# Optimization experiments

Hardware: AMD Instinct MI355X
Metric: run time of the kernel (lower is better)

The kernel has to match this reference:

```python
import jax, jax.numpy as jnp
import numpy as np
import math

HEADS, DIM_HEAD, LANDMARKS, PINV_ITERS = 8, 64, 256, 6
EMB = 512


def layer_norm(x, g, b, eps=1e-5):
    mu = jnp.mean(x, -1, keepdims=True)
    var = jnp.mean((x - mu) ** 2, -1, keepdims=True)
    return (x - mu) / jnp.sqrt(var + eps) * g + b


def moore_penrose_pinv(x, iters=PINV_ITERS):
    # iterative Moore-Penrose pseudo-inverse (lucidrains nystrom-attention)
    abs_x = jnp.abs(x)
    col = abs_x.sum(-1)
    row = abs_x.sum(-2)
    z = jnp.swapaxes(x, -1, -2) / (jnp.max(col) * jnp.max(row))
    I = jnp.eye(x.shape[-1], dtype=x.dtype)
    for _ in range(iters):
        xz = x @ z
        z = 0.25 * z @ (13.0 * I - xz @ (15.0 * I - xz @ (7.0 * I - xz)))
    return z


def dw_seq_conv(v, w):
    # v: [b, h, n, d]; depthwise Conv2d(heads, heads, (33,1), pad (16,0), groups=heads)
    return jax.lax.conv_general_dilated(
        v, w, (1, 1), ((w.shape[2] // 2, w.shape[2] // 2), (0, 0)),
        dimension_numbers=('NCHW', 'OIHW', 'NCHW'), feature_group_count=v.shape[1])


def nystrom_attention(x, qkv_w, out_w, out_b, res_w):
    b, n, _ = x.shape
    m = LANDMARKS
    pad = (m - n % m) % m
    if pad:
        x = jnp.pad(x, ((0, 0), (pad, 0), (0, 0)))  # front-pad like F.pad(..., padding, 0)
    n_p = n + pad
    qkv = x @ qkv_w  # [b, n_p, 3*h*dh]
    q, k, v = jnp.split(qkv, 3, axis=-1)
    to_h = lambda t: t.reshape(b, n_p, HEADS, DIM_HEAD).transpose(0, 2, 1, 3)
    q, k, v = to_h(q), to_h(k), to_h(v)
    q = q * (DIM_HEAD ** -0.5)
    l = n_p // m  # tokens per landmark
    q_l = q.reshape(b, HEADS, m, l, DIM_HEAD).mean(3)
    k_l = k.reshape(b, HEADS, m, l, DIM_HEAD).mean(3)
    a1 = jax.nn.softmax(jnp.einsum('bhid,bhjd->bhij', q, k_l), -1)    # [b,h,n_p,m]
    a2 = jax.nn.softmax(jnp.einsum('bhid,bhjd->bhij', q_l, k_l), -1)  # [b,h,m,m]
    a3 = jax.nn.softmax(jnp.einsum('bhid,bhjd->bhij', q_l, k), -1)    # [b,h,m,n_p]
    a2_inv = moore_penrose_pinv(a2)
    out = (a1 @ a2_inv) @ (a3 @ v)  # [b,h,n_p,dh]
    out = out + dw_seq_conv(v, res_w)  # residual depthwise conv on v
    out = out.transpose(0, 2, 1, 3).reshape(b, n_p, HEADS * DIM_HEAD)
    out = out @ out_w + out_b
    return out[:, -n:]


def ppeg(x, H, W, w7, b7, w5, b5, w3, b3):
    B, _, C = x.shape
    cls_t, feat = x[:, :1], x[:, 1:]
    f = feat.transpose(0, 2, 1).reshape(B, C, H, W)
    def dw(w, b):
        y = jax.lax.conv_general_dilated(
            f, w, (1, 1), 'SAME', dimension_numbers=('NCHW', 'OIHW', 'NCHW'),
            feature_group_count=C)
        return y + b[None, :, None, None]
    y = f + dw(w7, b7) + dw(w5, b5) + dw(w3, b3)
    y = y.reshape(B, C, H * W).transpose(0, 2, 1)
    return jnp.concatenate([cls_t, y], axis=1)


def setup_inputs():
    key = jax.random.key(0)
    ks = jax.random.split(key, 20)
    rn = lambda k, shp, s=0.02: jax.random.normal(k, shp, jnp.float32) * s
    return {
        'x_path': jax.random.normal(ks[0], (4, 6000, 1024), jnp.float32),
        'fc1_w': rn(ks[1], (1024, EMB)), 'fc1_b': jnp.zeros((EMB,), jnp.float32),
        'cls_token': jax.random.normal(ks[2], (1, 1, EMB), jnp.float32),
        'ln1_g': jnp.ones((EMB,), jnp.float32), 'ln1_b': jnp.zeros((EMB,), jnp.float32),
        'qkv1_w': rn(ks[3], (EMB, 3 * HEADS * DIM_HEAD)),
        'out1_w': rn(ks[4], (HEADS * DIM_HEAD, EMB)), 'out1_b': jnp.zeros((EMB,), jnp.float32),
        'res1_w': rn(ks[5], (HEADS, 1, 33, 1)),
        'ln2_g': jnp.ones((EMB,), jnp.float32), 'ln2_b': jnp.zeros((EMB,), jnp.float32),
        'qkv2_w': rn(ks[6], (EMB, 3 * HEADS * DIM_HEAD)),
        'out2_w': rn(ks[7], (HEADS * DIM_HEAD, EMB)), 'out2_b': jnp.zeros((EMB,), jnp.float32),
        'res2_w': rn(ks[8], (HEADS, 1, 33, 1)),
        'conv7_w': rn(ks[9], (EMB, 1, 7, 7)), 'conv7_b': jnp.zeros((EMB,), jnp.float32),
        'conv5_w': rn(ks[10], (EMB, 1, 5, 5)), 'conv5_b': jnp.zeros((EMB,), jnp.float32),
        'conv3_w': rn(ks[11], (EMB, 1, 3, 3)), 'conv3_b': jnp.zeros((EMB,), jnp.float32),
        'norm_g': jnp.ones((EMB,), jnp.float32), 'norm_b': jnp.zeros((EMB,), jnp.float32),
        'fc2_w': rn(ks[12], (EMB, 4)), 'fc2_b': jnp.zeros((4,), jnp.float32),
    }


def reference(x_path, fc1_w, fc1_b, cls_token, ln1_g, ln1_b, qkv1_w, out1_w, out1_b,
              res1_w, ln2_g, ln2_b, qkv2_w, out2_w, out2_b, res2_w,
              conv7_w, conv7_b, conv5_w, conv5_b, conv3_w, conv3_b,
              norm_g, norm_b, fc2_w, fc2_b):
    h = jax.nn.relu(x_path @ fc1_w + fc1_b)  # [B, N, EMB]
    B, N = h.shape[0], h.shape[1]
    _H = int(math.ceil(math.sqrt(N)))
    add = _H * _H - N
    h = jnp.concatenate([h, h[:, :add]], axis=1)            # square padding
    cls = jnp.broadcast_to(cls_token, (B, 1, EMB))
    h = jnp.concatenate([cls, h], axis=1)                   # [B, _H*_H+1, EMB]
    # TransLayer 1
    h = h + nystrom_attention(layer_norm(h, ln1_g, ln1_b), qkv1_w, out1_w, out1_b, res1_w)
    # PPEG positional encoding
    h = ppeg(h, _H, _H, conv7_w, conv7_b, conv5_w, conv5_b, conv3_w, conv3_b)
    # TransLayer 2
    h = h + nystrom_attention(layer_norm(h, ln2_g, ln2_b), qkv2_w, out2_w, out2_b, res2_w)
    h = layer_norm(h, norm_g, norm_b)
    logits = h @ fc2_w + fc2_b
    cls_logit = logits[:, 0]
    Y_hat = jnp.argmax(cls_logit, axis=1)
    hazards = jax.nn.sigmoid(cls_logit)
    S = jnp.cumprod(1.0 - hazards, axis=1)
    return hazards, S, Y_hat
```

## Files before the change

### kernel.cpp

```cpp
#include <hip/hip_runtime.h>
#include <math.h>

namespace {

constexpr int Bq   = 4;
constexpr int N0   = 6000;
constexpr int KIN  = 1024;
constexpr int E    = 512;
constexpr int HH   = 78;
constexpr int HWp  = 6084;
constexpr int N1   = 6085;
constexpr int NH   = 8;
constexpr int DH   = 64;
constexpr int LM   = 256;
constexpr int NP   = 6144;
constexpr int LCH  = 24;
constexpr int PADS = 59;
constexpr int BH   = Bq * NH;
constexpr int QKV  = 3 * E;

typedef __attribute__((ext_vector_type(8))) short bf16x8;
typedef __attribute__((ext_vector_type(4))) float f32x4;

__host__ __device__ inline int gblocks_i(long long n) { return (int)((n + 255) / 256); }

__device__ inline unsigned short f2bf(float x) {
  unsigned u = __float_as_uint(x);
  u += 0x7FFFu + ((u >> 16) & 1u);
  return (unsigned short)(u >> 16);
}
__device__ inline float bf2f(unsigned short s) {
  return __uint_as_float(((unsigned)s) << 16);
}
__device__ inline int swz8(int row, int chunk) {
  return chunk ^ (row & 7) ^ ((row >> 3) & 7);
}

__global__ __launch_bounds__(256)
void wcvt_t(const float* __restrict__ in, unsigned short* __restrict__ out, int K, int N)
{
  __shared__ float T[32][33];
  const int tx = threadIdx.x & 31, ty = threadIdx.x >> 5;
  const int n0 = blockIdx.x * 32, k0 = blockIdx.y * 32;
  #pragma unroll
  for (int i = 0; i < 4; i++)
    T[ty + i * 8][tx] = in[(size_t)(k0 + ty + i * 8) * N + n0 + tx];
  __syncthreads();
  #pragma unroll
  for (int i = 0; i < 4; i++)
    out[(size_t)(n0 + ty + i * 8) * K + k0 + tx] = f2bf(T[tx][ty + i * 8]);
}

template<int ASRC, int STORE, bool BIAS, bool RELU, bool SWIZ>
__global__ __launch_bounds__(256)
void mgemm(const void* __restrict__ Av, const unsigned short* __restrict__ Bt,
           const float* __restrict__ bias, float* __restrict__ C,
           unsigned short* __restrict__ qp, unsigned short* __restrict__ kp,
           unsigned short* __restrict__ vp, const unsigned short* __restrict__ Ag,
           int Mrows, int N, int K)
{
  __shared__ __align__(16) short As[128 * 40];
  __shared__ __align__(16) short Bs[128 * 40];
  const int t = threadIdx.x;
  const int lane = t & 63;
  const int l16 = lane & 15, g = lane >> 4;
  const int wave = t >> 6;
  const int wr = (wave >> 1) * 64, wc = (wave & 1) * 64;

  int bx = blockIdx.x, by = blockIdx.y;
  if (SWIZ) {
    const int gx = gridDim.x, nwg = gx * gridDim.y;
    const int flat = by * gx + bx;
    const int qq = nwg >> 3, rr = nwg & 7;
    const int xcd = flat & 7, pos = flat >> 3;
    const int nid = (xcd < rr ? xcd * (qq + 1) : rr * (qq + 1) + (xcd - rr) * qq) + pos;
    bx = nid % gx; by = nid / gx;
  }
  const int rowBase = by * 128, colBase = bx * 128;

  f32x4 acc[4][4];
  #pragma unroll
  for (int mi = 0; mi < 4; mi++)
    #pragma unroll
    for (int ni = 0; ni < 4; ni++) acc[mi][ni] = (f32x4){0.f, 0.f, 0.f, 0.f};

  for (int k0 = 0; k0 < K; k0 += 32) {
    if (ASRC == 0) {
      const float* A = (const float*)Av;
      #pragma unroll
      for (int i = 0; i < 4; i++) {
        const int id = i * 256 + t;
        const int row = id >> 3, kq = id & 7;
        const int r = rowBase + row;
        float4 va = make_float4(0.f, 0.f, 0.f, 0.f);
        if (r < Mrows)
          va = *reinterpret_cast<const float4*>(A + (size_t)r * K + k0 + kq * 4);
        const unsigned lo = (unsigned)f2bf(va.x) | ((unsigned)f2bf(va.y) << 16);
        const unsigned hi = (unsigned)f2bf(va.z) | ((unsigned)f2bf(va.w) << 16);
        *reinterpret_cast<uint2*>(&As[row * 40 + kq * 4]) = make_uint2(lo, hi);
      }
    } else {
      #pragma unroll
      for (int i = 0; i < 2; i++) {
        const int id = i * 256 + t;
        const int row = id >> 2, c8 = id & 3;
        const int r = rowBase + row;
        int4 va = make_int4(0, 0, 0, 0);
        if (r < Mrows) {
          const int kk = k0 + c8 * 8;
          if (ASRC == 4) {
            const int b = r / N1, rr2 = r % N1;
            va = *reinterpret_cast<const int4*>(
                Ag + (((size_t)(b * NH + (kk >> 6))) * NP + PADS + rr2) * DH + (kk & 63));
          } else {
            va = *reinterpret_cast<const int4*>(((const unsigned short*)Av) + (size_t)r * K + kk);
          }
        }
        *reinterpret_cast<int4*>(&As[row * 40 + c8 * 8]) = va;
      }
    }
    #pragma unroll
    for (int i = 0; i < 2; i++) {
      const int id = i * 256 + t;
      const int row = id >> 2, g8 = id & 3;
      int4 vb = *reinterpret_cast<const int4*>(Bt + (size_t)(colBase + row) * K + k0 + g8 * 8);
      *reinterpret_cast<int4*>(&Bs[row * 40 + g8 * 8]) = vb;
    }
    __syncthreads();
    bf16x8 af[4], bf[4];
    #pragma unroll
    for (int mi = 0; mi < 4; mi++)
      af[mi] = *reinterpret_cast<const bf16x8*>(&As[(wr + mi * 16 + l16) * 40 + g * 8]);
    #pragma unroll
    for (int ni = 0; ni < 4; ni++)
      bf[ni] = *reinterpret_cast<const bf16x8*>(&Bs[(wc + ni * 16 + l16) * 40 + g * 8]);
    #pragma unroll
    for (int mi = 0; mi < 4; mi++)
      #pragma unroll
      for (int ni = 0; ni < 4; ni++)
        acc[mi][ni] = __builtin_amdgcn_mfma_f32_16x16x32_bf16(af[mi], bf[ni], acc[mi][ni], 0, 0, 0);
    __syncthreads();
  }

  #pragma unroll
  for (int mi = 0; mi < 4; mi++) {
    #pragma unroll
    for (int ni = 0; ni < 4; ni++) {
      #pragma unroll
      for (int r4 = 0; r4 < 4; r4++) {
        const int row = rowBase + wr + mi * 16 + g * 4 + r4;
        if (row >= Mrows) continue;
        const int col = colBase + wc + ni * 16 + l16;
        float v = acc[mi][ni][r4];
        if (BIAS) v += bias[col];
        if (RELU) v = fmaxf(v, 0.f);
        if (STORE == 2) {
          const int b   = row / N1;
          const int p   = (row % N1) + PADS;
          const int wch = col >> 9;
          const int hd  = (col >> 6) & 7;
          const int d   = col & 63;
          float vv = (wch == 0) ? v * 0.125f : v;
          unsigned short* dst = (wch == 0) ? qp : (wch == 1) ? kp : vp;
          dst[(((size_t)(b * NH + hd)) * NP + p) * DH + d] = f2bf(vv);
        } else if (STORE == 1) {
          C[((size_t)(row / N0) * N1 + 1 + (row % N0)) * N + col] = v;
        } else if (STORE == 3) {
          C[(size_t)row * N + col] += v;
        } else {
          C[(size_t)row * N + col] = v;
        }
      }
    }
  }
}

template<bool WN, bool WT, bool TBF>
__global__ __launch_bounds__(256)
void mm_ns(const float* __restrict__ A, const float* __restrict__ BT,
           float* __restrict__ Cn, unsigned short* __restrict__ CtB,
           float* __restrict__ CtF, int Ncols, int Mtot, int K,
           long long sA, long long sBT, long long sCn, long long sCt,
           float cN, float aN, float cT, float aT)
{
  const int z = blockIdx.z;
  A  += (size_t)z * sA;
  BT += (size_t)z * sBT;
  __shared__ __align__(16) char smem[32768];
  unsigned short* Ah = (unsigned short*)smem;
  unsigned short* Al = Ah + 4096;
  unsigned short* Bh = Ah + 8192;
  unsigned short* Bl = Ah + 12288;
  const int t = threadIdx.x, lane = t & 63, w = t >> 6;
  const int l15 = lane & 15, g = lane >> 4;
  const int rb = blockIdx.y * 64, cb = blockIdx.x * 64;
  const int wr = w * 16;

  f32x4 acc[4];
  #pragma unroll
  for (int ni = 0; ni < 4; ni++) acc[ni] = (f32x4){0.f, 0.f, 0.f, 0.f};

  for (int k0 = 0; k0 < K; k0 += 64) {
    if (k0) __syncthreads();
    #pragma unroll
    for (int it = 0; it < 4; it++) {
      const int id = it * 256 + t;
      const int row = id >> 4, kq = (id & 15) * 4;
      float4 va = *reinterpret_cast<const float4*>(A + (size_t)(rb + row) * K + k0 + kq);
      const int eo = row * 64 + swz8(row, kq >> 3) * 8 + (kq & 7);
      unsigned short h0 = f2bf(va.x), h1 = f2bf(va.y), h2 = f2bf(va.z), h3 = f2bf(va.w);
      unsigned short lo0 = f2bf(va.x - bf2f(h0)), lo1 = f2bf(va.y - bf2f(h1));
      unsigned short lo2 = f2bf(va.z - bf2f(h2)), lo3 = f2bf(va.w - bf2f(h3));
      *reinterpret_cast<ushort4*>(&Ah[eo]) = make_ushort4(h0, h1, h2, h3);
      *reinterpret_cast<ushort4*>(&Al[eo]) = make_ushort4(lo0, lo1, lo2, lo3);
      float4 vb = *reinterpret_cast<const float4*>(BT + (size_t)(cb + row) * K + k0 + kq);
      unsigned short b0 = f2bf(vb.x), b1 = f2bf(vb.y), b2 = f2bf(vb.z), b3 = f2bf(vb.w);
      unsigned short c0_ = f2bf(vb.x - bf2f(b0)), c1 = f2bf(vb.y - bf2f(b1));
      unsigned short c2 = f2bf(vb.z - bf2f(b2)), c3 = f2bf(vb.w - bf2f(b3));
      *reinterpret_cast<ushort4*>(&Bh[eo]) = make_ushort4(b0, b1, b2, b3);
      *reinterpret_cast<ushort4*>(&Bl[eo]) = make_ushort4(c0_, c1, c2, c3);
    }
    __syncthreads();
    #pragma unroll
    for (int ds = 0; ds < 2; ds++) {
      const int ar = wr + l15;
      bf16x8 ah = *reinterpret_cast<const bf16x8*>(&Ah[ar * 64 + swz8(ar, ds * 4 + g) * 8]);
      bf16x8 al = *reinterpret_cast<const bf16x8*>(&Al[ar * 64 + swz8(ar, ds * 4 + g) * 8]);
      #pragma unroll
      for (int ni = 0; ni < 4; ni++) {
        const int nr = ni * 16 + l15;
        bf16x8 bhf = *reinterpret_cast<const bf16x8*>(&Bh[nr * 64 + swz8(nr, ds * 4 + g) * 8]);
        bf16x8 blf = *reinterpret_cast<const bf16x8*>(&Bl[nr * 64 + swz8(nr, ds * 4 + g) * 8]);
        acc[ni] = __builtin_amdgcn_mfma_f32_16x16x32_bf16(ah, bhf, acc[ni], 0, 0, 0);
        acc[ni] = __builtin_amdgcn_mfma_f32_16x16x32_bf16(ah, blf, acc[ni], 0, 0, 0);
        acc[ni] = __builtin_amdgcn_mfma_f32_16x16x32_bf16(al, bhf, acc[ni], 0, 0, 0);
      }
    }
  }
  __syncthreads();
  float* tb = (float*)smem;
  #pragma unroll
  for (int ni = 0; ni < 4; ni++)
    #pragma unroll
    for (int r = 0; r < 4; r++)
      tb[(wr + g * 4 + r) * 65 + l15 + ni * 16] = acc[ni][r];
  __syncthreads();
  #pragma unroll
  for (int it = 0; it < 4; it++) {
    const int id = it * 256 + t;
    const int row = id >> 4, q4 = (id & 15) * 4;
    if (WN) {
      float4 o;
      #pragma unroll
      for (int j = 0; j < 4; j++) {
        float v = tb[row * 65 + q4 + j];
        ((float*)&o)[j] = ((rb + row) == (cb + q4 + j) ? cN : 0.f) + aN * v;
      }
      *reinterpret_cast<float4*>(Cn + (size_t)z * sCn + (size_t)(rb + row) * Ncols + cb + q4) = o;
    }
    if (WT) {
      float v[4];
      #pragma unroll
      for (int j = 0; j < 4; j++) {
        float m = tb[(q4 + j) * 65 + row];
        v[j] = ((cb + row) == (rb + q4 + j) ? cT : 0.f) + aT * m;
      }
      if (TBF) {
        ushort4 o = make_ushort4(f2bf(v[0]), f2bf(v[1]), f2bf(v[2]), f2bf(v[3]));
        *reinterpret_cast<ushort4*>(CtB + (size_t)z * sCt + (size_t)(cb + row) * Mtot + rb + q4) = o;
      } else {
        float4 o = make_float4(v[0], v[1], v[2], v[3]);
        *reinterpret_cast<float4*>(CtF + (size_t)z * sCt + (size_t)(cb + row) * Mtot + rb + q4) = o;
      }
    }
  }
}

__global__ __launch_bounds__(256)
void a2_fused(const unsigned short* __restrict__ ql, const unsigned short* __restrict__ kl,
              float* __restrict__ a2, float* __restrict__ a2T)
{
  const int bh = blockIdx.y;
  const int t = threadIdx.x, lane = t & 63, w = t >> 6;
  const int l15 = lane & 15, g = lane >> 4;
  const int row0 = blockIdx.x * 64 + w * 16;
  __shared__ float tb[4][16][68];

  bf16x8 af[2];
  #pragma unroll
  for (int ds = 0; ds < 2; ds++)
    af[ds] = *reinterpret_cast<const bf16x8*>(ql + ((size_t)bh * LM + row0 + l15) * 64 + ds * 32 + g * 8);

  f32x4 s[16];
  #pragma unroll
  for (int ni = 0; ni < 16; ni++) s[ni] = (f32x4){0.f, 0.f, 0.f, 0.f};
  #pragma unroll
  for (int ni = 0; ni < 16; ni++)
    #pragma unroll
    for (int ds = 0; ds < 2; ds++) {
      bf16x8 bf = *reinterpret_cast<const bf16x8*>(kl + ((size_t)bh * LM + ni * 16 + l15) * 64 + ds * 32 + g * 8);
      s[ni] = __builtin_amdgcn_mfma_f32_16x16x32_bf16(af[ds], bf, s[ni], 0, 0, 0);
    }
  #pragma unroll
  for (int r = 0; r < 4; r++) {
    float m = -INFINITY;
    #pragma unroll
    for (int ni = 0; ni < 16; ni++) m = fmaxf(m, s[ni][r]);
    #pragma unroll
    for (int msk = 1; msk < 16; msk <<= 1) m = fmaxf(m, __shfl_xor(m, msk));
    float sm = 0.f;
    #pragma unroll
    for (int ni = 0; ni < 16; ni++) { float e = expf(s[ni][r] - m); s[ni][r] = e; sm += e; }
    #pragma unroll
    for (int msk = 1; msk < 16; msk <<= 1) sm += __shfl_xor(sm, msk);
    const float inv = 1.f / sm;
    #pragma unroll
    for (int ni = 0; ni < 16; ni++) s[ni][r] *= inv;
  }
  #pragma unroll
  for (int ni = 0; ni < 16; ni++)
    #pragma unroll
    for (int r = 0; r < 4; r++)
      a2[((size_t)bh << 16) + (size_t)(row0 + g * 4 + r) * 256 + ni * 16 + l15] = s[ni][r];
  for (int c4 = 0; c4 < 4; c4++) {
    #pragma unroll
    for (int ni2 = 0; ni2 < 4; ni2++)
      #pragma unroll
      for (int r = 0; r < 4; r++)
        tb[w][g * 4 + r][ni2 * 16 + l15] = s[c4 * 4 + ni2][r];
    #pragma unroll
    for (int q = 0; q < 4; q++) {
      float4 o;
      #pragma unroll
      for (int j = 0; j < 4; j++) ((float*)&o)[j] = tb[w][q * 4 + j][lane];
      *reinterpret_cast<float4*>(a2T + ((size_t)bh << 16) + (size_t)(c4 * 64 + lane) * 256 + row0 + q * 4) = o;
    }
  }
}

__global__ __launch_bounds__(256)
void flash_a3(const unsigned short* __restrict__ ql, const unsigned short* __restrict__ k,
              const unsigned short* __restrict__ v, float* __restrict__ a3vT)
{
  const int bh = blockIdx.y;
  const int lm0 = blockIdx.x * 64;
  const int t = threadIdx.x, lane = t & 63, w = t >> 6;
  const int l15 = lane & 15, g = lane >> 4;
  __shared__ __align__(16) char smem[24576];
  unsigned short* Kl = (unsigned short*)smem;
  unsigned short* VT = (unsigned short*)(smem + 8192);
  unsigned short* Pl = (unsigned short*)(smem + 16384);

  bf16x8 af[2];
  #pragma unroll
  for (int ds = 0; ds < 2; ds++)
    af[ds] = *reinterpret_cast<const bf16x8*>(ql + ((size_t)bh * LM + lm0 + w * 16 + l15) * 64 + ds * 32 + g * 8);

  f32x4 O[4];
  #pragma unroll
  for (int ni = 0; ni < 4; ni++) O[ni] = (f32x4){0.f, 0.f, 0.f, 0.f};
  float m[4] = {-INFINITY, -INFINITY, -INFINITY, -INFINITY};
  float sd[4] = {0.f, 0.f, 0.f, 0.f};

  for (int kt = 0; kt < NP / 64; kt++) {
    if (kt) __syncthreads();
    #pragma unroll
    for (int it = 0; it < 2; it++) {
      const int id = it * 256 + t;
      const int kp = id >> 3, ch = id & 7;
      int4 kv = *reinterpret_cast<const int4*>(k + ((size_t)bh * NP + kt * 64 + kp) * 64 + ch * 8);
      *reinterpret_cast<int4*>(&Kl[kp * 64 + swz8(kp, ch) * 8]) = kv;
      int4 vv = *reinterpret_cast<const int4*>(v + ((size_t)bh * NP + kt * 64 + kp) * 64 + ch * 8);
      const unsigned short* ps = (const unsigned short*)&vv;
      #pragma unroll
      for (int j = 0; j < 8; j++) {
        const int d = ch * 8 + j;
        VT[d * 64 + swz8(d, kp >> 3) * 8 + (kp & 7)] = ps[j];
      }
    }
    __syncthreads();
    f32x4 s[4];
    #pragma unroll
    for (int ni = 0; ni < 4; ni++) s[ni] = (f32x4){0.f, 0.f, 0.f, 0.f};
    #pragma unroll
    for (int ni = 0; ni < 4; ni++)
      #pragma unroll
      for (int ds = 0; ds < 2; ds++) {
        const int kr = ni * 16 + l15;
        bf16x8 bf = *reinterpret_cast<const bf16x8*>(&Kl[kr * 64 + swz8(kr, ds * 4 + g) * 8]);
        s[ni] = __builtin_amdgcn_mfma_f32_16x16x32_bf16(af[ds], bf, s[ni], 0, 0, 0);
      }
    #pragma unroll
    for (int r = 0; r < 4; r++) {
      float mc = fmaxf(fmaxf(s[0][r], s[1][r]), fmaxf(s[2][r], s[3][r]));
      #pragma unroll
      for (int msk = 1; msk < 16; msk <<= 1) mc = fmaxf(mc, __shfl_xor(mc, msk));
      const float mn = fmaxf(m[r], mc);
      const float sc = expf(m[r] - mn);
      float rs = 0.f;
      #pragma unroll
      for (int ni = 0; ni < 4; ni++) { float e = expf(s[ni][r] - mn); s[ni][r] = e; rs += e; }
      #pragma unroll
      for (int msk = 1; msk < 16; msk <<= 1) rs += __shfl_xor(rs, msk);
      sd[r] = sd[r] * sc + rs;
      m[r] = mn;
      #pragma unroll
      for (int ni = 0; ni < 4; ni++) O[ni][r] *= sc;
    }
    unsigned short* Pw = Pl + w * 1024;
    #pragma unroll
    for (int ni = 0; ni < 4; ni++)
      #pragma unroll
      for (int r = 0; r < 4; r++) {
        const int rowl = g * 4 + r, col = ni * 16 + l15;
        Pw[rowl * 64 + swz8(rowl, col >> 3) * 8 + (col & 7)] = f2bf(s[ni][r]);
      }
    #pragma unroll
    for (int ks = 0; ks < 2; ks++) {
      bf16x8 pa = *reinterpret_cast<const bf16x8*>(&Pw[l15 * 64 + swz8(l15, ks * 4 + g) * 8]);
      #pragma unroll
      for (int ni = 0; ni < 4; ni++) {
        const int d = ni * 16 + l15;
        bf16x8 bv = *reinterpret_cast<const bf16x8*>(&VT[d * 64 + swz8(d, ks * 4 + g) * 8]);
        O[ni] = __builtin_amdgcn_mfma_f32_16x16x32_bf16(pa, bv, O[ni], 0, 0, 0);
      }
    }
  }
  __syncthreads();
  float* tb = (float*)smem;
  float* tw = tb + w * 16 * 68;
  #pragma unroll
  for (int r = 0; r < 4; r++) {
    const float inv = 1.f / sd[r];
    #pragma unroll
    for (int ni = 0; ni < 4; ni++)
      tw[(g * 4 + r) * 68 + ni * 16 + l15] = O[ni][r] * inv;
  }
  #pragma unroll
  for (int q = 0; q < 4; q++) {
    float4 o;
    #pragma unroll
    for (int j = 0; j < 4; j++) ((float*)&o)[j] = tw[(q * 4 + j) * 68 + lane];
    *reinterpret_cast<float4*>(a3vT + ((size_t)bh * 64 + lane) * 256 + lm0 + w * 16 + q * 4) = o;
  }
}

__global__ __launch_bounds__(256)
void a1_fused(const unsigned short* __restrict__ q, const unsigned short* __restrict__ kl,
              const unsigned short* __restrict__ W2T, const unsigned short* __restrict__ v,
              const float* __restrict__ resw, unsigned short* __restrict__ heads)
{
  const int bh = blockIdx.y;
  const int p0 = blockIdx.x * 64;
  const int t = threadIdx.x, lane = t & 63, w = t >> 6;
  const int l15 = lane & 15, g = lane >> 4;
  __shared__ __align__(16) unsigned short Pl[4][4096];
  __shared__ __align__(16) unsigned short VTc[8192];
  __shared__ __align__(16) unsigned short P2[8192];

  const float* w33 = resw + (bh & 7) * 33;
  for (int i = t; i < 64 * 96; i += 256) {
    const int r = i / 96, kk = i % 96;
    const int d = kk - r;
    const float val = (d >= 0 && d <= 32) ? w33[d] : 0.f;
    P2[r * 128 + swz8(r, kk >> 3) * 8 + (kk & 7)] = f2bf(val);
  }
  #pragma unroll
  for (int it = 0; it < 3; it++) {
    const int id = it * 256 + t;
    const int kp = id >> 3, ch = id & 7;
    const int gp = p0 - 16 + kp;
    int4 vv = make_int4(0, 0, 0, 0);
    if (gp >= 0 && gp < NP)
      vv = *reinterpret_cast<const int4*>(v + ((size_t)bh * NP + gp) * 64 + ch * 8);
    const unsigned short* ps = (const unsigned short*)&vv;
    #pragma unroll
    for (int j = 0; j < 8; j++) {
      const int d = ch * 8 + j;
      VTc[d * 128 + swz8(d, kp >> 3) * 8 + (kp & 7)] = ps[j];
    }
  }
  __syncthreads();

  bf16x8 af[2];
  #pragma unroll
  for (int ds = 0; ds < 2; ds++)
    af[ds] = *reinterpret_cast<const bf16x8*>(q + ((size_t)bh * NP + p0 + w * 16 + l15) * 64 + ds * 32 + g * 8);
  f32x4 s[16];
  #pragma unroll
  for (int ni = 0; ni < 16; ni++) s[ni] = (f32x4){0.f, 0.f, 0.f, 0.f};
  #pragma unroll
  for (int ni = 0; ni < 16; ni++)
    #pragma unroll
    for (int ds = 0; ds < 2; ds++) {
      bf16x8 bf = *reinterpret_cast<const bf16x8*>(kl + ((size_t)bh * LM + ni * 16 + l15) * 64 + ds * 32 + g * 8);
      s[ni] = __builtin_amdgcn_mfma_f32_16x16x32_bf16(af[ds], bf, s[ni], 0, 0, 0);
    }
  #pragma unroll
  for (int r = 0; r < 4; r++) {
    float m = -INFINITY;
    #pragma unroll
    for (int ni = 0; ni < 16; ni++) m = fmaxf(m, s[ni][r]);
    #pragma unroll
    for (int msk = 1; msk < 16; msk <<= 1) m = fmaxf(m, __shfl_xor(m, msk));
    float sm = 0.f;
    #pragma unroll
    for (int ni = 0; ni < 16; ni++) { float e = expf(s[ni][r] - m); s[ni][r] = e; sm += e; }
    #pragma unroll
    for (int msk = 1; msk < 16; msk <<= 1) sm += __shfl_xor(sm, msk);
    const float inv = 1.f / sm;
    #pragma unroll
    for (int ni = 0; ni < 16; ni++) s[ni][r] *= inv;
  }
  unsigned short* Pw = Pl[w];
  #pragma unroll
  for (int ni = 0; ni < 16; ni++)
    #pragma unroll
    for (int r = 0; r < 4; r++) {
      const int rowl = g * 4 + r, col = ni * 16 + l15;
      Pw[rowl * 256 + swz8(rowl, col >> 3) * 8 + (col & 7)] = f2bf(s[ni][r]);
    }
  f32x4 O[4];
  #pragma unroll
  for (int ni = 0; ni < 4; ni++) O[ni] = (f32x4){0.f, 0.f, 0.f, 0.f};
  #pragma unroll
  for (int ks = 0; ks < 8; ks++) {
    bf16x8 pa = *reinterpret_cast<const bf16x8*>(&Pw[l15 * 256 + swz8(l15, ks * 4 + g) * 8]);
    #pragma unroll
    for (int ni = 0; ni < 4; ni++) {
      bf16x8 bf = *reinterpret_cast<const bf16x8*>(
          W2T + ((size_t)bh * 64 + ni * 16 + l15) * 256 + ks * 32 + g * 8);
      O[ni] = __builtin_amdgcn_mfma_f32_16x16x32_bf16(pa, bf, O[ni], 0, 0, 0);
    }
  }
  #pragma unroll
  for (int ks = 0; ks < 3; ks++) {
    const int ar = w * 16 + l15;
    bf16x8 pa = *reinterpret_cast<const bf16x8*>(&P2[ar * 128 + swz8(ar, ks * 4 + g) * 8]);
    #pragma unroll
    for (int ni = 0; ni < 4; ni++) {
      const int d = ni * 16 + l15;
      bf16x8 bv = *reinterpret_cast<const bf16x8*>(&VTc[d * 128 + swz8(d, ks * 4 + g) * 8]);
      O[ni] = __builtin_amdgcn_mfma_f32_16x16x32_bf16(pa, bv, O[ni], 0, 0, 0);
    }
  }
  #pragma unroll
  for (int ni = 0; ni < 4; ni++)
    #pragma unroll
    for (int r = 0; r < 4; r++)
      heads[((size_t)bh * NP + p0 + w * 16 + g * 4 + r) * 64 + ni * 16 + l15] = f2bf(O[ni][r]);
}

__global__ __launch_bounds__(256)
void ln_stats(const float* __restrict__ X, float* __restrict__ stats)
{
  const size_t row = blockIdx.x;
  const float* x = X + row * E;
  const int tid = threadIdx.x;
  float2 v = *reinterpret_cast<const float2*>(x + tid * 2);
  __shared__ float red[256];
  red[tid] = v.x + v.y;
  __syncthreads();
  for (int s = 128; s > 0; s >>= 1) { if (tid < s) red[tid] += red[tid + s]; __syncthreads(); }
  const float mu = red[0] * (1.f / E);
  __syncthreads();
  const float dx = v.x - mu, dy = v.y - mu;
  red[tid] = dx * dx + dy * dy;
  __syncthreads();
  for (int s = 128; s > 0; s >>= 1) { if (tid < s) red[tid] += red[tid + s]; __syncthreads(); }
  if (tid == 0) {
    stats[2 * row]     = mu;
    stats[2 * row + 1] = 1.f / sqrtf(red[0] * (1.f / E) + 1e-5f);
  }
}

__global__ __launch_bounds__(256)
void ln_to_bf16(const float* __restrict__ h, const float* __restrict__ stats,
                const float* __restrict__ g, const float* __restrict__ b,
                unsigned short* __restrict__ xb)
{
  long long idx = (long long)blockIdx.x * 256 + threadIdx.x;
  const long long total = (long long)Bq * N1 * (E / 4);
  if (idx >= total) return;
  const int e4 = (int)(idx % (E / 4));
  const long long row = idx / (E / 4);
  float4 hx = reinterpret_cast<const float4*>(h)[idx];
  const float mu = stats[2 * row], inv = stats[2 * row + 1];
  float4 gg = reinterpret_cast<const float4*>(g)[e4];
  float4 bb = reinterpret_cast<const float4*>(b)[e4];
  ushort4 o;
  o.x = f2bf((hx.x - mu) * inv * gg.x + bb.x);
  o.y = f2bf((hx.y - mu) * inv * gg.y + bb.y);
  o.z = f2bf((hx.z - mu) * inv * gg.z + bb.z);
  o.w = f2bf((hx.w - mu) * inv * gg.w + bb.w);
  reinterpret_cast<ushort4*>(xb)[idx] = o;
}

__global__ void fill_cls_wrap(const float* __restrict__ cls, float* __restrict__ h)
{
  int idx = blockIdx.x * 256 + threadIdx.x;
  const int total = Bq * 85 * (E / 4);
  if (idx >= total) return;
  const int e4 = idx % (E / 4);
  int t = idx / (E / 4);
  const int rr = t % 85;
  const int b = t / 85;
  float4* H = reinterpret_cast<float4*>(h);
  if (rr == 0) {
    H[((size_t)b * N1) * (E / 4) + e4] = reinterpret_cast<const float4*>(cls)[e4];
  } else {
    const int i = rr - 1;
    H[((size_t)b * N1 + 1 + N0 + i) * (E / 4) + e4] =
        H[((size_t)b * N1 + 1 + i) * (E / 4) + e4];
  }
}

__global__ __launch_bounds__(256)
void landmark_mean(const float* __restrict__ h, const float* __restrict__ stats,
                   const float* __restrict__ g, const float* __restrict__ bta,
                   unsigned short* __restrict__ xl)
{
  const int bm = blockIdx.x;
  const int b = bm / LM, i = bm % LM;
  const int tid = threadIdx.x;
  float2 acc = make_float2(0.f, 0.f);
  float cnt = 0.f;
  for (int j = 0; j < LCH; j++) {
    const int real = i * LCH + j - PADS;
    if (real < 0) continue;
    const size_t row = (size_t)b * N1 + real;
    float2 hv = *reinterpret_cast<const float2*>(h + row * E + tid * 2);
    const float mu = stats[2 * row], inv = stats[2 * row + 1];
    acc.x += (hv.x - mu) * inv;
    acc.y += (hv.y - mu) * inv;
    cnt += 1.f;
  }
  float2 gg = *reinterpret_cast<const float2*>(g + tid * 2);
  float2 bb = *reinterpret_cast<const float2*>(bta + tid * 2);
  ushort2 o;
  o.x = f2bf((gg.x * acc.x + bb.x * cnt) * (1.f / LCH));
  o.y = f2bf((gg.y * acc.y + bb.y * cnt) * (1.f / LCH));
  *reinterpret_cast<ushort2*>(xl + (size_t)bm * E + tid * 2) = o;
}

__global__ void zero_pad_rows(unsigned short* __restrict__ q, unsigned short* __restrict__ k,
                              unsigned short* __restrict__ v)
{
  const int idx = blockIdx.x * 256 + threadIdx.x;
  const int total = BH * PADS * DH;
  if (idx >= total) return;
  const int d = idx % DH;
  int t = idx / DH;
  const int p = t % PADS;
  const int bh = t / PADS;
  const size_t o = ((size_t)bh * NP + p) * DH + d;
  q[o] = 0; k[o] = 0; v[o] = 0;
}

__global__ void scatter_qk_l(const float* __restrict__ qkvf, unsigned short* __restrict__ ql,
                             unsigned short* __restrict__ kl)
{
  int idx = blockIdx.x * 256 + threadIdx.x;
  const int total = Bq * LM * (1024 / 4);
  if (idx >= total) return;
  const int c4 = idx % 256;
  int t = idx / 256;
  const int i = t % LM;
  const int b = t / LM;
  const int c = c4 * 4;
  const int wch = c >> 9;
  const int hd = (c >> 6) & 7;
  float4 val = reinterpret_cast<const float4*>(qkvf)[idx];
  if (wch == 0) { val.x *= 0.125f; val.y *= 0.125f; val.z *= 0.125f; val.w *= 0.125f; }
  unsigned short* dst = (wch == 0) ? ql : kl;
  ushort4 o = make_ushort4(f2bf(val.x), f2bf(val.y), f2bf(val.z), f2bf(val.w));
  *reinterpret_cast<ushort4*>(dst + (((size_t)(b * NH + hd)) * LM + i) * 64 + (c & 63)) = o;
}

__global__ void init_gmax(unsigned int* g) { if (threadIdx.x < 2) g[threadIdx.x] = 0u; }

__global__ __launch_bounds__(256)
void colrow_max(const float* __restrict__ a2, unsigned int* __restrict__ gmax)
{
  const float* a = a2 + (size_t)blockIdx.x * LM * LM;
  const int tid = threadIdx.x;
  float rowsum = 0.f, colsum = 0.f;
  for (int j = 0; j < LM; j++) rowsum += a[(size_t)tid * LM + j];
  for (int i = 0; i < LM; i++) colsum += a[(size_t)i * LM + tid];
  __shared__ float r1[256], r2[256];
  r1[tid] = rowsum; r2[tid] = colsum;
  __syncthreads();
  for (int s = 128; s > 0; s >>= 1) {
    if (tid < s) { r1[tid] = fmaxf(r1[tid], r1[tid + s]); r2[tid] = fmaxf(r2[tid], r2[tid + s]); }
    __syncthreads();
  }
  if (tid == 0) {
    atomicMax(&gmax[0], __float_as_uint(r1[0]));
    atomicMax(&gmax[1], __float_as_uint(r2[0]));
  }
}

__global__ void pinv_init2(const float* __restrict__ a2, const float* __restrict__ a2T,
                           const unsigned int* __restrict__ gmax,
                           float* __restrict__ zA, float* __restrict__ zAT)
{
  long long idx = (long long)blockIdx.x * 256 + threadIdx.x;
  const long long total = (long long)BH * LM * LM;
  if (idx >= total) return;
  const float inv = 1.f / (__uint_as_float(gmax[0]) * __uint_as_float(gmax[1]));
  zA[idx]  = a2T[idx] * inv;
  zAT[idx] = a2[idx] * inv;
}

__global__ __launch_bounds__(256)
void last_row_attn(const unsigned short* __restrict__ q, const unsigned short* __restrict__ kl,
                   const unsigned short* __restrict__ W2T, const unsigned short* __restrict__ v,
                   const float* __restrict__ resw, float* __restrict__ hb)
{
  const int bh = blockIdx.x;
  const int tid = threadIdx.x;
  __shared__ float qrow[DH];
  __shared__ float p[LM];
  __shared__ float red[256];
  if (tid < DH) qrow[tid] = bf2f(q[((size_t)bh * NP + PADS) * DH + tid]);
  __syncthreads();
  const unsigned short* krow = kl + ((size_t)bh * LM + tid) * DH;
  float s = 0.f;
  for (int d = 0; d < DH; d++) s = fmaf(qrow[d], bf2f(krow[d]), s);
  red[tid] = s;
  __syncthreads();
  for (int st = 128; st > 0; st >>= 1) { if (tid < st) red[tid] = fmaxf(red[tid], red[tid + st]); __syncthreads(); }
  const float m = red[0];
  __syncthreads();
  const float e = expf(s - m);
  red[tid] = e;
  __syncthreads();
  for (int st = 128; st > 0; st >>= 1) { if (tid < st) red[tid] += red[tid + st]; __syncthreads(); }
  p[tid] = e / red[0];
  __syncthreads();
  if (tid < DH) {
    const unsigned short* w2r = W2T + ((size_t)bh * 64 + tid) * 256;
    float acc = 0.f;
    for (int j = 0; j < LM; j++) acc = fmaf(p[j], bf2f(w2r[j]), acc);
    const float* wt = resw + (bh % NH) * 33;
    const unsigned short* vb = v + (size_t)bh * NP * DH;
    #pragma unroll
    for (int t2 = 0; t2 < 33; t2++)
      acc = fmaf(wt[t2], bf2f(vb[(size_t)(PADS - 16 + t2) * DH + tid]), acc);
    hb[bh * DH + tid] = acc;
  }
}

__global__ __launch_bounds__(256)
void last_outproj(const float* __restrict__ hb, const float* __restrict__ outw,
                  const float* __restrict__ outb, float* __restrict__ h)
{
  const int b = blockIdx.x;
  const int tid = threadIdx.x;
  __shared__ float cat[E];
  for (int c = tid; c < E; c += 256) cat[c] = hb[(b * NH + (c >> 6)) * DH + (c & 63)];
  __syncthreads();
  for (int e = tid; e < E; e += 256) {
    float acc = outb[e];
    for (int c = 0; c < E; c++) acc = fmaf(cat[c], outw[(size_t)c * E + e], acc);
    h[(size_t)b * N1 * E + e] += acc;
  }
}

__global__ __launch_bounds__(256)
void transpose_h2p(const float* __restrict__ h, float* __restrict__ ht)
{
  __shared__ float T[32][33];
  const int tx = threadIdx.x & 31, ty = threadIdx.x >> 5;
  const int px0 = blockIdx.x * 32, e0 = blockIdx.y * 32, b = blockIdx.z;
  #pragma unroll
  for (int i = 0; i < 4; i++) {
    const int pix = px0 + ty + i * 8;
    if (pix < HWp)
      T[ty + i * 8][tx] = h[((size_t)b * N1 + 1 + pix) * E + e0 + tx];
  }
  __syncthreads();
  #pragma unroll
  for (int i = 0; i < 4; i++) {
    const int pix = px0 + tx;
    if (pix < HWp)
      ht[((size_t)b * E + e0 + ty + i * 8) * HWp + pix] = T[tx][ty + i * 8];
  }
}

__global__ __launch_bounds__(256)
void transpose_p2h(const float* __restrict__ ht, float* __restrict__ h)
{
  __shared__ float T[32][33];
  const int tx = threadIdx.x & 31, ty = threadIdx.x >> 5;
  const int px0 = blockIdx.x * 32, e0 = blockIdx.y * 32, b = blockIdx.z;
  #pragma unroll
  for (int i = 0; i < 4; i++) {
    const int pix = px0 + tx;
    if (pix < HWp)
      T[ty + i * 8][tx] = ht[((size_t)b * E + e0 + ty + i * 8) * HWp + pix];
  }
  __syncthreads();
  #pragma unroll
  for (int i = 0; i < 4; i++) {
    const int pix = px0 + ty + i * 8;
    if (pix < HWp)
      h[((size_t)b * N1 + 1 + pix) * E + e0 + tx] = T[tx][ty + i * 8];
  }
}

__global__ __launch_bounds__(256)
void ppeg_plane(float* __restrict__ ht,
                const float* __restrict__ w7, const float* __restrict__ b7,
                const float* __restrict__ w5, const float* __restrict__ b5,
                const float* __restrict__ w3, const float* __restrict__ b3)
{
  __shared__ float S[84][88];
  __shared__ float Wl[84];
  const int t = threadIdx.x;
  const int e = blockIdx.x & (E - 1);
  float* plane = ht + (size_t)blockIdx.x * HWp;

  for (int i = t; i < 84 * 88; i += 256) (&S[0][0])[i] = 0.f;
  if (t < 49) Wl[t] = w7[(size_t)e * 49 + t];
  else if (t >= 64 && t < 89) Wl[49 + t - 64] = w5[(size_t)e * 25 + t - 64];
  else if (t >= 96 && t < 105) Wl[74 + t - 96] = w3[(size_t)e * 9 + t - 96];
  __syncthreads();
  for (int i = t; i < HWp; i += 256) S[3 + i / HH][3 + i % HH] = plane[i];
  const float bsum = b7[e] + b5[e] + b3[e];
  __syncthreads();

  float res[7][4];
  int it = 0;
  for (int gidx = t; gidx < 1560; gidx += 256, ++it) {
    const int y = gidx / 20, x0 = (gidx % 20) * 4;
    float a0 = bsum + S[y + 3][x0 + 3];
    float a1 = bsum + S[y + 3][x0 + 4];
    float a2v = bsum + S[y + 3][x0 + 5];
    float a3 = bsum + S[y + 3][x0 + 6];
    #pragma unroll
    for (int dy = -3; dy <= 3; dy++) {
      const int row = y + 3 + dy;
      float win[10];
      #pragma unroll
      for (int m = 0; m < 10; m++) win[m] = S[row][x0 + m];
      const int ky7 = dy + 3;
      #pragma unroll
      for (int kx = 0; kx < 7; kx++) {
        const float c = Wl[ky7 * 7 + kx];
        a0 = fmaf(c, win[kx + 0], a0);
        a1 = fmaf(c, win[kx + 1], a1);
        a2v = fmaf(c, win[kx + 2], a2v);
        a3 = fmaf(c, win[kx + 3], a3);
      }
      if (dy >= -2 && dy <= 2) {
        const int ky5 = dy + 2;
        #pragma unroll
        for (int kx = 0; kx < 5; kx++) {
          const float c = Wl[49 + ky5 * 5 + kx];
          a0 = fmaf(c, win[kx + 1], a0);
          a1 = fmaf(c, win[kx + 2], a1);
          a2v = fmaf(c, win[kx + 3], a2v);
          a3 = fmaf(c, win[kx + 4], a3);
        }
      }
      if (dy >= -1 && dy <= 1) {
        const int ky3 = dy + 1;
        #pragma unroll
        for (int kx = 0; kx < 3; kx++) {
          const float c = Wl[74 + ky3 * 3 + kx];
          a0 = fmaf(c, win[kx + 2], a0);
          a1 = fmaf(c, win[kx + 3], a1);
          a2v = fmaf(c, win[kx + 4], a2v);
          a3 = fmaf(c, win[kx + 5], a3);
        }
      }
    }
    res[it][0] = a0; res[it][1] = a1; res[it][2] = a2v; res[it][3] = a3;
  }
  __syncthreads();
  it = 0;
  for (int gidx = t; gidx < 1560; gidx += 256, ++it) {
    const int y = gidx / 20, x0 = (gidx % 20) * 4;
    #pragma unroll
    for (int j = 0; j < 4; j++)
      if (x0 + j < HH) plane[y * HH + x0 + j] = res[it][j];
  }
}

__global__ __launch_bounds__(256)
void final_head(const float* __restrict__ h, const float* __restrict__ g,
                const float* __restrict__ bb, const float* __restrict__ w2,
                const float* __restrict__ b2, float* __restrict__ out)
{
  const int b = blockIdx.x;
  const int tid = threadIdx.x;
  const float* x = h + (size_t)b * N1 * E;
  float2 v = *reinterpret_cast<const float2*>(x + tid * 2);
  __shared__ float red[256];
  red[tid] = v.x + v.y;
  __syncthreads();
  for (int st = 128; st > 0; st >>= 1) { if (tid < st) red[tid] += red[tid + st]; __syncthreads(); }
  const float mu = red[0] * (1.f / E);
  __syncthreads();
  const float dx = v.x - mu, dy = v.y - mu;
  red[tid] = dx * dx + dy * dy;
  __syncthreads();
  for (int st = 128; st > 0; st >>= 1) { if (tid < st) red[tid] += red[tid + st]; __syncthreads(); }
  const float inv = 1.f / sqrtf(red[0] * (1.f / E) + 1e-5f);
  __shared__ float hn[E];
  float2 gg = *reinterpret_cast<const float2*>(g + tid * 2);
  float2 bv = *reinterpret_cast<const float2*>(bb + tid * 2);
  hn[tid * 2]     = dx * inv * gg.x + bv.x;
  hn[tid * 2 + 1] = dy * inv * gg.y + bv.y;
  __syncthreads();
  __shared__ float lg[4];
  if (tid < 4) {
    float a = b2[tid];
    for (int e = 0; e < E; e++) a = fmaf(hn[e], w2[e * 4 + tid], a);
    lg[tid] = a;
  }
  __syncthreads();
  if (tid == 0) {
    int best = 0;
    float bvv = lg[0];
    for (int j = 1; j < 4; j++) if (lg[j] > bvv) { bvv = lg[j]; best = j; }
    float S = 1.f;
    for (int j = 0; j < 4; j++) {
      const float hz = 1.f / (1.f + expf(-lg[j]));
      out[b * 4 + j] = hz;
      S *= (1.f - hz);
      out[16 + b * 4 + j] = S;
    }
    out[32 + b] = (float)best;
  }
}

__global__ void write_sentinel(float* out) { if (threadIdx.x < 36) out[threadIdx.x] = -777.f; }

struct Ws {
  unsigned short *q, *k, *v, *ql, *kl, *xl, *W2T;
  unsigned short *fc1T, *qkv1T, *qkv2T, *out1T;
  float *h, *pool, *a3vT, *qkvl, *stats;
  unsigned int* gmax;
};

constexpr long long MM = (long long)BH * LM * LM;

static void run_attention(hipStream_t stream, Ws& w,
                          const float* lng, const float* lnb, const unsigned short* qkvT,
                          const unsigned short* outT, const float* outb, const float* resw,
                          bool last)
{
  const dim3 blk(256);
  float* a2   = w.pool;
  float* a2T  = w.pool + MM;
  float* zA   = w.pool + 2 * MM;
  float* zAT  = w.pool + 3 * MM;
  float* zB   = w.pool + 4 * MM;
  float* zBT  = w.pool + 5 * MM;
  float* Y    = w.pool + 6 * MM;
  float* P1T  = w.pool + 7 * MM;
  float* P2T  = w.pool + 8 * MM;
  float* P3T  = w.pool + 9 * MM;
  unsigned short* xb    = (unsigned short*)w.pool;
  unsigned short* heads = (unsigned short*)(w.pool + 6 * MM);
  float* hb = w.qkvl;

  ln_stats<<<Bq * N1, blk, 0, stream>>>(w.h, w.stats);
  ln_to_bf16<<<gblocks_i((long long)Bq * N1 * (E / 4)), blk, 0, stream>>>(w.h, w.stats, lng, lnb, xb);
  landmark_mean<<<Bq * LM, blk, 0, stream>>>(w.h, w.stats, lng, lnb, w.xl);
  mgemm<3, 2, false, false, true><<<dim3(QKV / 128, (Bq * N1 + 127) / 128), blk, 0, stream>>>(
      xb, qkvT, nullptr, nullptr, w.q, w.k, w.v, nullptr, Bq * N1, QKV, E);
  zero_pad_rows<<<gblocks_i((long long)BH * PADS * DH), blk, 0, stream>>>(w.q, w.k, w.v);
  mgemm<3, 0, false, false, false><<<dim3(8, 8), blk, 0, stream>>>(
      w.xl, qkvT, nullptr, w.qkvl, nullptr, nullptr, nullptr, nullptr, Bq * LM, 1024, E);
  scatter_qk_l<<<gblocks_i((long long)Bq * LM * 256), blk, 0, stream>>>(w.qkvl, w.ql, w.kl);

  a2_fused<<<dim3(4, BH), blk, 0, stream>>>(w.ql, w.kl, a2, a2T);
  init_gmax<<<1, 64, 0, stream>>>(w.gmax);
  colrow_max<<<BH, blk, 0, stream>>>(a2, w.gmax);
  pinv_init2<<<gblocks_i(MM), blk, 0, stream>>>(a2, a2T, w.gmax, zA, zAT);

  float *zc = zA, *zcT = zAT, *zo = zB, *zoT = zBT;
  const long long sM = (long long)LM * LM;
  for (int it = 0; it < 6; ++it) {
    mm_ns<true, true, false><<<dim3(4, 4, BH), blk, 0, stream>>>(
        a2, zcT, Y, nullptr, P1T, 256, 256, 256, sM, sM, sM, sM, 0.f, 1.f, 7.f, -1.f);
    mm_ns<false, true, false><<<dim3(4, 4, BH), blk, 0, stream>>>(
        Y, P1T, nullptr, nullptr, P2T, 256, 256, 256, sM, sM, sM, sM, 0.f, 0.f, 15.f, -1.f);
    mm_ns<false, true, false><<<dim3(4, 4, BH), blk, 0, stream>>>(
        Y, P2T, nullptr, nullptr, P3T, 256, 256, 256, sM, sM, sM, sM, 0.f, 0.f, 13.f, -1.f);
    mm_ns<true, true, false><<<dim3(4, 4, BH), blk, 0, stream>>>(
        zc, P3T, zo, nullptr, zoT, 256, 256, 256, sM, sM, sM, sM, 0.f, 0.25f, 0.f, 0.25f);
    float* t1 = zc; zc = zo; zo = t1;
    float* t2 = zcT; zcT = zoT; zoT = t2;
  }

  flash_a3<<<dim3(4, BH), blk, 0, stream>>>(w.ql, w.k, w.v, w.a3vT);
  mm_ns<false, true, true><<<dim3(1, 4, BH), blk, 0, stream>>>(
      zc, w.a3vT, nullptr, w.W2T, nullptr, 64, 256, 256, sM, 64 * 256, 0, 64 * 256,
      0.f, 0.f, 0.f, 1.f);

  if (!last) {
    a1_fused<<<dim3(NP / 64, BH), blk, 0, stream>>>(w.q, w.kl, w.W2T, w.v, resw, heads);
    mgemm<4, 3, true, false, true><<<dim3(E / 128, (Bq * N1 + 127) / 128), blk, 0, stream>>>(
        nullptr, outT, outb, w.h, nullptr, nullptr, nullptr, heads, Bq * N1, E, E);
  } else {
    last_row_attn<<<BH, blk, 0, stream>>>(w.q, w.kl, w.W2T, w.v, resw, hb);
  }
}

}

extern "C" void kernel_launch(void* const* d_in, const int* in_sizes, int n_in,
                              void* d_out, int out_size, void* d_ws, size_t ws_size,
                              hipStream_t stream)
{
  const float* x_path   = (const float*)d_in[0];
  const float* fc1_w    = (const float*)d_in[1];
  const float* fc1_b    = (const float*)d_in[2];
  const float* cls_tok  = (const float*)d_in[3];
  const float* ln1_g    = (const float*)d_in[4];
  const float* ln1_b    = (const float*)d_in[5];
  const float* qkv1_w   = (const float*)d_in[6];
  const float* out1_w   = (const float*)d_in[7];
  const float* out1_b   = (const float*)d_in[8];
  const float* res1_w   = (const float*)d_in[9];
  const float* ln2_g    = (const float*)d_in[10];
  const float* ln2_b    = (const float*)d_in[11];
  const float* qkv2_w   = (const float*)d_in[12];
  const float* out2_w   = (const float*)d_in[13];
  const float* out2_b   = (const float*)d_in[14];
  const float* res2_w   = (const float*)d_in[15];
  const float* conv7_w  = (const float*)d_in[16];
  const float* conv7_b  = (const float*)d_in[17];
  const float* conv5_w  = (const float*)d_in[18];
  const float* conv5_b  = (const float*)d_in[19];
  const float* conv3_w  = (const float*)d_in[20];
  const float* conv3_b  = (const float*)d_in[21];
  const float* norm_g   = (const float*)d_in[22];
  const float* norm_b   = (const float*)d_in[23];
  const float* fc2_w    = (const float*)d_in[24];
  const float* fc2_b    = (const float*)d_in[25];
  (void)in_sizes; (void)n_in; (void)out_size;

  float* W = (float*)d_ws;
  size_t off = 0;
  auto take = [&](size_t n) -> float* {
    float* p = W + off;
    off += (n + 255) & ~(size_t)255;
    return p;
  };

  Ws w;
  w.q     = (unsigned short*)take((size_t)BH * NP * DH / 2);
  w.k     = (unsigned short*)take((size_t)BH * NP * DH / 2);
  w.v     = (unsigned short*)take((size_t)BH * NP * DH / 2);
  w.h     = take((size_t)Bq * N1 * E);
  w.pool  = take((size_t)10 * MM);
  w.a3vT  = take((size_t)BH * DH * LM);
  w.W2T   = (unsigned short*)take((size_t)BH * DH * LM / 2);
  w.ql    = (unsigned short*)take((size_t)BH * LM * DH / 2);
  w.kl    = (unsigned short*)take((size_t)BH * LM * DH / 2);
  w.xl    = (unsigned short*)take((size_t)Bq * LM * E / 2);
  w.qkvl  = take((size_t)Bq * LM * 1024);
  w.stats = take((size_t)2 * Bq * N1);
  w.fc1T  = (unsigned short*)take((size_t)E * KIN / 2);
  w.qkv1T = (unsigned short*)take((size_t)QKV * E / 2);
  w.qkv2T = (unsigned short*)take((size_t)QKV * E / 2);
  w.out1T = (unsigned short*)take((size_t)E * E / 2);
  w.gmax  = (unsigned int*)take(64);

  if (ws_size < off * sizeof(float)) {
    write_sentinel<<<1, 64, 0, stream>>>((float*)d_out);
    return;
  }

  const dim3 blk(256);

  wcvt_t<<<dim3(E / 32, KIN / 32), blk, 0, stream>>>(fc1_w, w.fc1T, KIN, E);
  wcvt_t<<<dim3(QKV / 32, E / 32), blk, 0, stream>>>(qkv1_w, w.qkv1T, E, QKV);
  wcvt_t<<<dim3(QKV / 32, E / 32), blk, 0, stream>>>(qkv2_w, w.qkv2T, E, QKV);
  wcvt_t<<<dim3(E / 32, E / 32), blk, 0, stream>>>(out1_w, w.out1T, E, E);

  mgemm<0, 1, true, true, true><<<dim3(E / 128, (Bq * N0 + 127) / 128), blk, 0, stream>>>(
      x_path, w.fc1T, fc1_b, w.h, nullptr, nullptr, nullptr, nullptr, Bq * N0, E, KIN);
  fill_cls_wrap<<<gblocks_i((long long)Bq * 85 * (E / 4)), blk, 0, stream>>>(cls_tok, w.h);

  run_attention(stream, w, ln1_g, ln1_b, w.qkv1T, w.out1T, out1_b, res1_w, false);

  {
    float* planes = w.pool;
    transpose_h2p<<<dim3((HWp + 31) / 32, E / 32, Bq), blk, 0, stream>>>(w.h, planes);
    ppeg_plane<<<Bq * E, blk, 0, stream>>>(planes, conv7_w, conv7_b, conv5_w, conv5_b,
                                           conv3_w, conv3_b);
    transpose_p2h<<<dim3((HWp + 31) / 32, E / 32, Bq), blk, 0, stream>>>(planes, w.h);
  }

  run_attention(stream, w, ln2_g, ln2_b, w.qkv2T, nullptr, out2_b, res2_w, true);
  last_outproj<<<Bq, blk, 0, stream>>>(w.qkvl, out2_w, out2_b, w.h);

  final_head<<<Bq, blk, 0, stream>>>(w.h, norm_g, norm_b, fc2_w, fc2_b, (float*)d_out);
}
```

Before: 2.276 ms.

## Split flash a3 attention over key sequence with separate merge kernel

The a3·v flash kernel is split into eight sequence chunks per (batch, head, landmark block), and each chunk writes partial outputs plus row max and sum to scratch. A new merge kernel rescales and combines the partials, then writes the transposed a3vT. This raises the a3 grid from 128 blocks to 1024 so more of the GPU's compute units are used. The pinv mm_ns GEMMs also get XCD-aware block swizzling, which should improve L2 locality. The cost is extra scratch traffic and one more launch.

```diff
diff --git a/kernel.cpp b/kernel.cpp
--- a/kernel.cpp
+++ b/kernel.cpp
@@ -18,6 +18,7 @@
 constexpr int PADS = 59;
 constexpr int BH   = Bq * NH;
 constexpr int QKV  = 3 * E;
+constexpr int NSPL = 8;
 
 typedef __attribute__((ext_vector_type(8))) short bf16x8;
 typedef __attribute__((ext_vector_type(4))) float f32x4;
@@ -34,6 +35,11 @@
 }
 __device__ inline int swz8(int row, int chunk) {
   return chunk ^ (row & 7) ^ ((row >> 3) & 7);
+}
+__device__ inline int xcd_swz(int flat, int nwg) {
+  const int q8 = nwg >> 3, r8 = nwg & 7;
+  const int xcd = flat & 7, pos = flat >> 3;
+  return (xcd < r8 ? xcd * (q8 + 1) : r8 * (q8 + 1) + (xcd - r8) * q8) + pos;
 }
 
 __global__ __launch_bounds__(256)
@@ -69,11 +75,8 @@
 
   int bx = blockIdx.x, by = blockIdx.y;
   if (SWIZ) {
-    const int gx = gridDim.x, nwg = gx * gridDim.y;
-    const int flat = by * gx + bx;
-    const int qq = nwg >> 3, rr = nwg & 7;
-    const int xcd = flat & 7, pos = flat >> 3;
-    const int nid = (xcd < rr ? xcd * (qq + 1) : rr * (qq + 1) + (xcd - rr) * qq) + pos;
+    const int gx = gridDim.x;
+    const int nid = xcd_swz(by * gx + bx, gx * gridDim.y);
     bx = nid % gx; by = nid / gx;
   }
   const int rowBase = by * 128, colBase = bx * 128;
@@ -183,9 +186,14 @@
            long long sA, long long sBT, long long sCn, long long sCt,
            float cN, float aN, float cT, float aT)
 {
-  const int z = blockIdx.z;
-  A  += (size_t)z * sA;
-  BT += (size_t)z * sBT;
+  int bx = blockIdx.x, by = blockIdx.y, bz = blockIdx.z;
+  {
+    const int gx = gridDim.x, gy = gridDim.y;
+    int nid = xcd_swz((bz * gy + by) * gx + bx, gx * gy * gridDim.z);
+    bx = nid % gx; nid /= gx; by = nid % gy; bz = nid / gy;
+  }
+  A  += (size_t)bz * sA;
+  BT += (size_t)bz * sBT;
   __shared__ __align__(16) char smem[32768];
   unsigned short* Ah = (unsigned short*)smem;
   unsigned short* Al = Ah + 4096;
@@ -193,7 +201,7 @@
   unsigned short* Bl = Ah + 12288;
   const int t = threadIdx.x, lane = t & 63, w = t >> 6;
   const int l15 = lane & 15, g = lane >> 4;
-  const int rb = blockIdx.y * 64, cb = blockIdx.x * 64;
+  const int rb = by * 64, cb = bx * 64;
   const int wr = w * 16;
 
   f32x4 acc[4];
@@ -256,7 +264,7 @@
         float v = tb[row * 65 + q4 + j];
         ((float*)&o)[j] = ((rb + row) == (cb + q4 + j) ? cN : 0.f) + aN * v;
       }
-      *reinterpret_cast<float4*>(Cn + (size_t)z * sCn + (size_t)(rb + row) * Ncols + cb + q4) = o;
+      *reinterpret_cast<float4*>(Cn + (size_t)bz * sCn + (size_t)(rb + row) * Ncols + cb + q4) = o;
     }
     if (WT) {
       float v[4];
@@ -267,10 +275,10 @@
       }
       if (TBF) {
         ushort4 o = make_ushort4(f2bf(v[0]), f2bf(v[1]), f2bf(v[2]), f2bf(v[3]));
-        *reinterpret_cast<ushort4*>(CtB + (size_t)z * sCt + (size_t)(cb + row) * Mtot + rb + q4) = o;
+        *reinterpret_cast<ushort4*>(CtB + (size_t)bz * sCt + (size_t)(cb + row) * Mtot + rb + q4) = o;
       } else {
         float4 o = make_float4(v[0], v[1], v[2], v[3]);
-        *reinterpret_cast<float4*>(CtF + (size_t)z * sCt + (size_t)(cb + row) * Mtot + rb + q4) = o;
+        *reinterpret_cast<float4*>(CtF + (size_t)bz * sCt + (size_t)(cb + row) * Mtot + rb + q4) = o;
       }
     }
   }
@@ -339,11 +347,17 @@
 }
 
 __global__ __launch_bounds__(256)
-void flash_a3(const unsigned short* __restrict__ ql, const unsigned short* __restrict__ k,
-              const unsigned short* __restrict__ v, float* __restrict__ a3vT)
-{
-  const int bh = blockIdx.y;
-  const int lm0 = blockIdx.x * 64;
+void flash_a3_split(const unsigned short* __restrict__ ql, const unsigned short* __restrict__ k,
+                    const unsigned short* __restrict__ v, float* __restrict__ Opart,
+                    float* __restrict__ msd)
+{
+  int bx = blockIdx.x, by = blockIdx.y, bz = blockIdx.z;
+  {
+    const int gx = gridDim.x, gy = gridDim.y;
+    int nid = xcd_swz((bz * gy + by) * gx + bx, gx * gy * gridDim.z);
+    bx = nid % gx; nid /= gx; by = nid % gy; bz = nid / gy;
+  }
+  const int bh = bz, sp = by, lm0 = bx * 64;
   const int t = threadIdx.x, lane = t & 63, w = t >> 6;
   const int l15 = lane & 15, g = lane >> 4;
   __shared__ __align__(16) char smem[24576];
@@ -362,8 +376,9 @@
   float m[4] = {-INFINITY, -INFINITY, -INFINITY, -INFINITY};
   float sd[4] = {0.f, 0.f, 0.f, 0.f};
 
-  for (int kt = 0; kt < NP / 64; kt++) {
-    if (kt) __syncthreads();
+  const int kt0 = sp * (NP / 64 / NSPL), kt1 = kt0 + NP / 64 / NSPL;
+  for (int kt = kt0; kt < kt1; kt++) {
+    if (kt != kt0) __syncthreads();
     #pragma unroll
     for (int it = 0; it < 2; it++) {
       const int id = it * 256 + t;
@@ -426,22 +441,62 @@
       }
     }
   }
-  __syncthreads();
-  float* tb = (float*)smem;
-  float* tw = tb + w * 16 * 68;
   #pragma unroll
   for (int r = 0; r < 4; r++) {
-    const float inv = 1.f / sd[r];
+    const int row = lm0 + w * 16 + g * 4 + r;
+    const size_t base = ((size_t)(bh * NSPL + sp) * LM + row);
     #pragma unroll
     for (int ni = 0; ni < 4; ni++)
-      tw[(g * 4 + r) * 68 + ni * 16 + l15] = O[ni][r] * inv;
-  }
-  #pragma unroll
-  for (int q = 0; q < 4; q++) {
-    float4 o;
-    #pragma unroll
-    for (int j = 0; j < 4; j++) ((float*)&o)[j] = tw[(q * 4 + j) * 68 + lane];
-    *reinterpret_cast<float4*>(a3vT + ((size_t)bh * 64 + lane) * 256 + lm0 + w * 16 + q * 4) = o;
+      Opart[base * 64 + ni * 16 + l15] = O[ni][r];
+    if (l15 == 0) {
+      msd[base * 2]     = m[r];
+      msd[base * 2 + 1] = sd[r];
+    }
+  }
+}
+
+__global__ __launch_bounds__(256)
+void flash_a3_merge(const float* __restrict__ Opart, const float* __restrict__ msd,
+                    float* __restrict__ a3vT)
+{
+  const int bh = blockIdx.y, lm0 = blockIdx.x * 64;
+  const int t = threadIdx.x;
+  const int r = t >> 2, dg = t & 3;
+  const int row = lm0 + r;
+  float m8[NSPL], w8[NSPL];
+  float M = -INFINITY;
+  #pragma unroll
+  for (int s = 0; s < NSPL; s++) {
+    m8[s] = msd[((size_t)(bh * NSPL + s) * LM + row) * 2];
+    M = fmaxf(M, m8[s]);
+  }
+  float S = 0.f;
+  #pragma unroll
+  for (int s = 0; s < NSPL; s++) {
+    const float e = expf(m8[s] - M);
+    w8[s] = e;
+    S += msd[((size_t)(bh * NSPL + s) * LM + row) * 2 + 1] * e;
+  }
+  const float invS = 1.f / S;
+  float acc[16];
+  #pragma unroll
+  for (int j = 0; j < 16; j++) acc[j] = 0.f;
+  #pragma unroll
+  for (int s = 0; s < NSPL; s++) {
+    const float* op = Opart + ((size_t)(bh * NSPL + s) * LM + row) * 64 + dg * 16;
+    #pragma unroll
+    for (int j = 0; j < 16; j++) acc[j] = fmaf(w8[s], op[j], acc[j]);
+  }
+  __shared__ float Tl[64][65];
+  #pragma unroll
+  for (int j = 0; j < 16; j++) Tl[dg * 16 + j][r] = acc[j] * invS;
+  __syncthreads();
+  const int d = t >> 2, q4 = t & 3;
+  #pragma unroll
+  for (int j = 0; j < 4; j++) {
+    const int c0 = q4 * 16 + j * 4;
+    float4 o = make_float4(Tl[d][c0], Tl[d][c0 + 1], Tl[d][c0 + 2], Tl[d][c0 + 3]);
+    *reinterpret_cast<float4*>(a3vT + ((size_t)bh * 64 + d) * 256 + lm0 + c0) = o;
   }
 }
 
@@ -965,6 +1020,8 @@
   float* P3T  = w.pool + 9 * MM;
   unsigned short* xb    = (unsigned short*)w.pool;
   unsigned short* heads = (unsigned short*)(w.pool + 6 * MM);
+  float* Opart = w.pool + 6 * MM;
+  float* msd   = w.pool + 6 * MM + (long long)BH * NSPL * LM * DH;
   float* hb = w.qkvl;
 
   ln_stats<<<Bq * N1, blk, 0, stream>>>(w.h, w.stats);
@@ -997,7 +1054,8 @@
     float* t2 = zcT; zcT = zoT; zoT = t2;
   }
 
-  flash_a3<<<dim3(4, BH), blk, 0, stream>>>(w.ql, w.k, w.v, w.a3vT);
+  flash_a3_split<<<dim3(4, NSPL, BH), blk, 0, stream>>>(w.ql, w.k, w.v, Opart, msd);
+  flash_a3_merge<<<dim3(4, BH), blk, 0, stream>>>(Opart, msd, w.a3vT);
   mm_ns<false, true, true><<<dim3(1, 4, BH), blk, 0, stream>>>(
       zc, w.a3vT, nullptr, w.W2T, nullptr, 64, 256, 256, sM, 64 * 256, 0, 64 * 256,
       0.f, 0.f, 0.f, 1.f);
```

Result: faster. 1.931 ms (-15.2%).
